# Kernel tuning notes

Measured on AMD Instinct MI355X. Metric: run time of the kernel, lower is better.

## Reference

```python
import jax, jax.numpy as jnp
import numpy as np

L, H, D, E, F, T, B, V = 6, 6, 64, 384, 1536, 256, 256, 65


def setup_inputs() -> dict:
    key = jax.random.key(0)
    ks = iter(jax.random.split(key, 32))
    s = 0.02
    n = lambda shape: jax.random.normal(next(ks), shape, dtype=jnp.float32) * s
    inp = {
        "inputs": jax.random.randint(next(ks), (B, T), 0, V),
        "targets": jax.random.randint(next(ks), (B, T), 0, V),
        "tok_emb": n((V, E)),
        "pos_emb": n((T, E)),
        "Wq": n((L, H, E, D)),
        "Wk": n((L, H, E, D)),
        "Wv": n((L, H, E, D)),
        "Wo": n((L, E, E)),
        "bo": jnp.zeros((L, E), jnp.float32),
        "ln1_g": jnp.ones((L, E), jnp.float32),
        "ln1_b": jnp.zeros((L, E), jnp.float32),
        "W1": n((L, E, F)),
        "b1": jnp.zeros((L, F), jnp.float32),
        "W2": n((L, F, E)),
        "b2": jnp.zeros((L, E), jnp.float32),
        "ln2_g": jnp.ones((L, E), jnp.float32),
        "ln2_b": jnp.zeros((L, E), jnp.float32),
        "lnf_g": jnp.ones((E,), jnp.float32),
        "lnf_b": jnp.zeros((E,), jnp.float32),
        "Wh": n((E, V)),
        "bh": jnp.zeros((V,), jnp.float32),
    }
    return inp


def _layer_norm(x, g, b, eps=1e-5):
    mu = jnp.mean(x, axis=-1, keepdims=True)
    var = jnp.var(x, axis=-1, keepdims=True)
    return (x - mu) * jax.lax.rsqrt(var + eps) * g + b


def _forward(inputs, targets, tok_emb, pos_emb, Wq, Wk, Wv, Wo, bo,
             ln1_g, ln1_b, W1, b1, W2, b2, ln2_g, ln2_b, lnf_g, lnf_b, Wh, bh):
    Bc, Tc = inputs.shape
    x = tok_emb[inputs] + pos_emb[:Tc]  # [B,T,E]
    causal = jnp.tril(jnp.ones((Tc, Tc), bool))
    scale = D ** -0.5
    for l in range(L):
        h = _layer_norm(x, ln1_g[l], ln1_b[l])
        q = jnp.einsum('bte,hed->bhtd', h, Wq[l])
        k = jnp.einsum('bte,hed->bhtd', h, Wk[l])
        v = jnp.einsum('bte,hed->bhtd', h, Wv[l])
        scores = jnp.einsum('bhtd,bhsd->bhts', q, k) * scale
        scores = jnp.where(causal, scores, -jnp.inf)
        att = jax.nn.softmax(scores, axis=-1)
        o = jnp.einsum('bhts,bhsd->bhtd', att, v)
        o = o.transpose(0, 2, 1, 3).reshape(Bc, Tc, E)  # concat heads
        x = x + o @ Wo[l] + bo[l]
        h2 = _layer_norm(x, ln2_g[l], ln2_b[l])
        x = x + jax.nn.relu(h2 @ W1[l] + b1[l]) @ W2[l] + b2[l]
    x = _layer_norm(x, lnf_g, lnf_b)
    logits = x @ Wh + bh  # [B,T,V]
    logp = jax.nn.log_softmax(logits, axis=-1)
    nll = -jnp.take_along_axis(logp, targets[..., None], axis=-1)[..., 0]
    loss = jnp.mean(nll)
    return logits.reshape(Bc * Tc, V), loss


def reference(inputs, targets, tok_emb, pos_emb, Wq, Wk, Wv, Wo, bo,
              ln1_g, ln1_b, W1, b1, W2, b2, ln2_g, ln2_b, lnf_g, lnf_b, Wh, bh):
    return _forward(inputs, targets, tok_emb, pos_emb, Wq, Wk, Wv, Wo, bo,
                    ln1_g, ln1_b, W1, b1, W2, b2, ln2_g, ln2_b, lnf_g, lnf_b, Wh, bh)
```

## Files before the change

kernel.cpp:

```cpp
#include <hip/hip_runtime.h>
#include <math.h>

#define LL 6
#define HH 6
#define EE 384
#define FF 1536
#define TT 256
#define BB 256
#define VV 65
constexpr int BT = BB * TT;

typedef __attribute__((ext_vector_type(8))) short s16x8;
typedef __attribute__((ext_vector_type(4))) float f32x4;
typedef __attribute__((ext_vector_type(2))) unsigned int u32x2;
typedef unsigned int uint;
typedef unsigned short ushort_t;

__device__ __forceinline__ float uaf(uint u) { union { uint u; float f; } c; c.u = u; return c.f; }
__device__ __forceinline__ ushort_t f2b(float f) {
  union { float f; uint u; } c; c.f = f;
  uint r = c.u + 0x7fffu + ((c.u >> 16) & 1u);
  return (ushort_t)(r >> 16);
}
__device__ __forceinline__ float b2f(ushort_t b) { return uaf((uint)b << 16); }

__device__ __forceinline__ void gload_lds16(const void* g, void* l) {
  __builtin_amdgcn_global_load_lds(
      (const __attribute__((address_space(1))) unsigned int*)g,
      (__attribute__((address_space(3))) unsigned int*)l, 16, 0, 0);
}

__global__ __launch_bounds__(256)
void embed_kernel(const int* __restrict__ inp, const float* __restrict__ tok,
                  const float* __restrict__ pos, float* __restrict__ x) {
  int idx = blockIdx.x * 256 + threadIdx.x;
  int e4 = idx % (EE / 4);
  int r = idx / (EE / 4);
  int t = r % TT;
  int tk = inp[r];
  float4 a = ((const float4*)tok)[tk * (EE / 4) + e4];
  float4 p = ((const float4*)pos)[t * (EE / 4) + e4];
  float4 o;
  o.x = a.x + p.x; o.y = a.y + p.y; o.z = a.z + p.z; o.w = a.w + p.w;
  ((float4*)x)[idx] = o;
}

__global__ __launch_bounds__(256)
void pack_qkv(const float* __restrict__ Wq, const float* __restrict__ Wk,
              const float* __restrict__ Wv, ushort_t* __restrict__ dst) {
  int idx = blockIdx.x * 256 + threadIdx.x;
  int l = idx / (1152 * 384);
  int r = idx % (1152 * 384);
  int n = r / 384;
  int k = r % 384;
  int which = n / 384;
  int hd = n % 384;
  int h = hd >> 6, d = hd & 63;
  const float* src = which == 0 ? Wq : (which == 1 ? Wk : Wv);
  dst[idx] = f2b(src[((size_t)(l * HH + h) * EE + k) * 64 + d]);
}

__global__ __launch_bounds__(256)
void pack_wt(const float* __restrict__ src, ushort_t* __restrict__ dst, int Kd, int Nd) {
  int idx = blockIdx.x * 256 + threadIdx.x;
  int l = idx / (Kd * Nd);
  int r = idx % (Kd * Nd);
  int n = r / Kd;
  int k = r % Kd;
  dst[idx] = f2b(src[((size_t)l * Kd + k) * Nd + n]);
}

__global__ __launch_bounds__(256)
void pack_head(const float* __restrict__ Wh, ushort_t* __restrict__ dst) {
  int idx = blockIdx.x * 256 + threadIdx.x;
  int n = idx / 384, k = idx % 384;
  dst[idx] = (n < VV) ? f2b(Wh[(size_t)k * VV + n]) : (ushort_t)0;
}

__global__ __launch_bounds__(256)
void layernorm_384(const float* __restrict__ x, const float* __restrict__ g,
                   const float* __restrict__ b, ushort_t* __restrict__ outp) {
  int wid = threadIdx.x >> 6, lane = threadIdx.x & 63;
  int row = blockIdx.x * 4 + wid;
  const float* xr = x + (size_t)row * EE;
  float v[6];
  float s = 0.f, s2 = 0.f;
#pragma unroll
  for (int i = 0; i < 6; ++i) {
    v[i] = xr[lane + 64 * i];
    s += v[i];
    s2 += v[i] * v[i];
  }
#pragma unroll
  for (int off = 32; off; off >>= 1) {
    s += __shfl_xor(s, off);
    s2 += __shfl_xor(s2, off);
  }
  float mu = s * (1.f / EE);
  float var = s2 * (1.f / EE) - mu * mu;
  float rs = rsqrtf(var + 1e-5f);
#pragma unroll
  for (int i = 0; i < 6; ++i) {
    int e = lane + 64 * i;
    outp[(size_t)row * EE + e] = f2b((v[i] - mu) * rs * g[e] + b[e]);
  }
}

__global__ __launch_bounds__(256)
void ln_res_384(float* __restrict__ x, const ushort_t* __restrict__ delta,
                const float* __restrict__ g, const float* __restrict__ b,
                ushort_t* __restrict__ outp) {
  int wid = threadIdx.x >> 6, lane = threadIdx.x & 63;
  int row = blockIdx.x * 4 + wid;
  float* xr = x + (size_t)row * EE;
  const ushort_t* dr = delta + (size_t)row * EE;
  float v[6];
  float s = 0.f, s2 = 0.f;
#pragma unroll
  for (int i = 0; i < 6; ++i) {
    int e = lane + 64 * i;
    v[i] = xr[e] + b2f(dr[e]);
    s += v[i];
    s2 += v[i] * v[i];
  }
#pragma unroll
  for (int off = 32; off; off >>= 1) {
    s += __shfl_xor(s, off);
    s2 += __shfl_xor(s2, off);
  }
  float mu = s * (1.f / EE);
  float var = s2 * (1.f / EE) - mu * mu;
  float rs = rsqrtf(var + 1e-5f);
#pragma unroll
  for (int i = 0; i < 6; ++i) {
    int e = lane + 64 * i;
    xr[e] = v[i];
    outp[(size_t)row * EE + e] = f2b((v[i] - mu) * rs * g[e] + b[e]);
  }
}

template <int MODE, bool BIAS, bool RELU>
__global__ __launch_bounds__(256)
void gemm_bf16(const ushort_t* __restrict__ A, const ushort_t* __restrict__ Wt,
               const float* __restrict__ bias, ushort_t* __restrict__ Cb,
               float* __restrict__ Cf, ushort_t* __restrict__ Cv,
               int M, int N, int K, int nx) {
  __shared__ ushort_t sm[16896];
  ushort_t* As = sm;
  ushort_t* Bs = sm + 8192;
  const int tid = threadIdx.x;

  int bid = blockIdx.x;
  {
    const int nwg = gridDim.x;
    const int q = nwg >> 3, rr = nwg & 7;
    const int xcd = bid & 7, within = bid >> 3;
    bid = (xcd < rr ? xcd * (q + 1) : rr * (q + 1) + (xcd - rr) * q) + within;
  }
  const int bn = (bid % nx) * 128;
  const int bm = (bid / nx) * 128;

  const int w = tid >> 6, lane = tid & 63;
  const int wr = (w >> 1) * 64, wc = (w & 1) * 64;
  const int fr = lane & 15, fq = lane >> 4;

  const int rp = lane >> 2;
  const int fqs = (lane & 3) ^ ((rp >> 1) & 3);
  const ushort_t* Ag0 = A + (size_t)(bm + w * 16 + rp) * K + fqs * 8;
  const ushort_t* Ag1 = Ag0 + (size_t)64 * K;
  const ushort_t* Bg0 = Wt + (size_t)(bn + w * 16 + rp) * K + fqs * 8;
  const ushort_t* Bg1 = Bg0 + (size_t)64 * K;

  const int slotr = (fq ^ ((fr >> 1) & 3)) * 8;
  const ushort_t* Ard = As + (wr + fr) * 32 + slotr;
  const ushort_t* Brd = Bs + (wc + fr) * 32 + slotr;

  const int nt = K >> 5;
  auto STAGE = [&](int kt, int b) {
    const int k0 = kt << 5;
    const int bo = b << 12;
    gload_lds16(Ag0 + k0, As + bo + (w * 16) * 32);
    gload_lds16(Ag1 + k0, As + bo + (64 + w * 16) * 32);
    gload_lds16(Bg0 + k0, Bs + bo + (w * 16) * 32);
    gload_lds16(Bg1 + k0, Bs + bo + (64 + w * 16) * 32);
  };

  f32x4 acc[4][4] = {};
  STAGE(0, 0);

  for (int t = 0; t < nt; ++t) {
    const int bo = (t & 1) << 12;
    if (t + 1 < nt) {
      STAGE(t + 1, (t & 1) ^ 1);
      asm volatile("s_waitcnt vmcnt(4)" ::: "memory");
    } else {
      asm volatile("s_waitcnt vmcnt(0)" ::: "memory");
    }
    __builtin_amdgcn_s_barrier();
    __builtin_amdgcn_sched_barrier(0);
    s16x8 afr[4], bfr[4];
#pragma unroll
    for (int m = 0; m < 4; ++m) afr[m] = *(const s16x8*)(Ard + bo + m * 512);
#pragma unroll
    for (int n = 0; n < 4; ++n) bfr[n] = *(const s16x8*)(Brd + bo + n * 512);
#pragma unroll
    for (int m = 0; m < 4; ++m)
#pragma unroll
      for (int n = 0; n < 4; ++n)
        acc[m][n] = __builtin_amdgcn_mfma_f32_16x16x32_bf16(afr[m], bfr[n], acc[m][n], 0, 0, 0);
    __builtin_amdgcn_sched_barrier(0);
    __builtin_amdgcn_s_barrier();
  }

  if constexpr (MODE == 0 || MODE == 3) {
    if (MODE == 3 && bn >= 768) {
      const int r0 = bm + wr + fq * 4;
      const int c0 = bn + wc + fr;
#pragma unroll
      for (int n = 0; n < 4; ++n) {
        const int col = c0 + n * 16 - 768;
#pragma unroll
        for (int m = 0; m < 4; ++m) {
          const int row = r0 + m * 16;
          uint lo = (uint)f2b(acc[m][n][0]) | ((uint)f2b(acc[m][n][1]) << 16);
          uint hi = (uint)f2b(acc[m][n][2]) | ((uint)f2b(acc[m][n][3]) << 16);
          *(u32x2*)&Cv[(size_t)col * M + row] = u32x2{lo, hi};
        }
      }
      return;
    }
    const int ostride = (MODE == 3) ? 768 : N;
#pragma unroll
    for (int n = 0; n < 4; ++n) {
      const int col = wc + n * 16 + fr;
      const float bv = BIAS ? bias[bn + col] : 0.f;
#pragma unroll
      for (int m = 0; m < 4; ++m) {
        const int row = wr + m * 16 + fq * 4;
#pragma unroll
        for (int j = 0; j < 4; ++j) {
          float vv = acc[m][n][j] + bv;
          if constexpr (RELU) vv = fmaxf(vv, 0.f);
          sm[(row + j) * 132 + col] = f2b(vv);
        }
      }
    }
    __syncthreads();
    const int rr2 = tid >> 4, cb = (tid & 15) * 8;
#pragma unroll
    for (int pp = 0; pp < 8; ++pp) {
      const int row = pp * 16 + rr2;
      s16x8 v8 = *(const s16x8*)(sm + row * 132 + cb);
      *(s16x8*)(Cb + (size_t)(bm + row) * ostride + bn + cb) = v8;
    }
    return;
  }
  const int r0 = bm + wr + fq * 4;
  const int c0 = bn + wc + fr;
#pragma unroll
  for (int n = 0; n < 4; ++n) {
    const int col = c0 + n * 16;
    if (col >= VV) continue;
    const float bv = BIAS ? bias[col] : 0.f;
#pragma unroll
    for (int m = 0; m < 4; ++m) {
      const int row = r0 + m * 16;
#pragma unroll
      for (int j = 0; j < 4; ++j)
        Cf[(size_t)(row + j) * VV + col] = acc[m][n][j] + bv;
    }
  }
}

__global__ __launch_bounds__(256)
void attn_kernel(const ushort_t* __restrict__ qk, const ushort_t* __restrict__ vt,
                 ushort_t* __restrict__ o, int R) {
  __shared__ ushort_t Ks[256 * 64];
  __shared__ ushort_t Pb[4][16 * 40];
  const int tid = threadIdx.x;
  const int w = tid >> 6, lane = tid & 63;
  const int seq = blockIdx.x / HH, hh = blockIdx.x % HH;
  const int brow = seq * TT;

  {
    const ushort_t* kbase = qk + (size_t)brow * 768 + 384 + hh * 64;
#pragma unroll
    for (int cc = 0; cc < 8; ++cc) {
      const int ci = cc * 256 + tid;
      const int s = ci >> 3, j = ci & 7;
      const int srcb = (j * 16) ^ ((s & 7) << 4);
      gload_lds16(kbase + (size_t)s * 768 + (srcb >> 1), Ks + cc * 2048 + w * 512);
    }
  }
  __syncthreads();

  const int r = lane & 15, g = lane >> 4;
  ushort_t* pw = &Pb[w][0];

  for (int fi = 0; fi < 4; ++fi) {
    const int q0 = fi * 64 + w * 16;
    const int n_st = (q0 >> 4) + 1;
    const ushort_t* qrow = qk + (size_t)(brow + q0 + r) * 768 + hh * 64 + g * 8;
    const s16x8 qa0 = *(const s16x8*)qrow;
    const s16x8 qa1 = *(const s16x8*)(qrow + 32);

    f32x4 S[16];
#pragma unroll
    for (int st = 0; st < 16; ++st) {
      if (st < n_st) {
        const int srow = st * 16 + r;
        const int sw = (srow & 7) << 4;
        const s16x8 kb0 = *(const s16x8*)(Ks + ((srow * 128 + ((g * 16) ^ sw)) >> 1));
        const s16x8 kb1 = *(const s16x8*)(Ks + ((srow * 128 + ((64 + g * 16) ^ sw)) >> 1));
        f32x4 t = {0.f, 0.f, 0.f, 0.f};
        t = __builtin_amdgcn_mfma_f32_16x16x32_bf16(qa0, kb0, t, 0, 0, 0);
        t = __builtin_amdgcn_mfma_f32_16x16x32_bf16(qa1, kb1, t, 0, 0, 0);
        if (st == n_st - 1) {
#pragma unroll
          for (int j = 0; j < 4; ++j)
            t[j] = (r <= g * 4 + j) ? t[j] : -1e30f;
        }
        S[st] = t;
      }
    }

    float mrow[4] = {-1e30f, -1e30f, -1e30f, -1e30f};
#pragma unroll
    for (int st = 0; st < 16; ++st)
      if (st < n_st) {
#pragma unroll
        for (int j = 0; j < 4; ++j) mrow[j] = fmaxf(mrow[j], S[st][j]);
      }
#pragma unroll
    for (int j = 0; j < 4; ++j) {
      float m = mrow[j];
      m = fmaxf(m, __shfl_xor(m, 1));
      m = fmaxf(m, __shfl_xor(m, 2));
      m = fmaxf(m, __shfl_xor(m, 4));
      m = fmaxf(m, __shfl_xor(m, 8));
      mrow[j] = m;
    }

    float rsum[4] = {0.f, 0.f, 0.f, 0.f};
    f32x4 O[4] = {f32x4{0,0,0,0}, f32x4{0,0,0,0}, f32x4{0,0,0,0}, f32x4{0,0,0,0}};
    const int n_sc = (n_st + 1) >> 1;
    const ushort_t* vbase = vt + (size_t)(hh * 64 + r) * R + brow + g * 8;
#pragma unroll
    for (int sc = 0; sc < 8; ++sc) {
      if (sc < n_sc) {
#pragma unroll
        for (int tt = 0; tt < 2; ++tt) {
          const int st = sc * 2 + tt;
#pragma unroll
          for (int j = 0; j < 4; ++j) {
            float p = 0.f;
            if (st < n_st) p = __expf((S[st][j] - mrow[j]) * 0.125f);
            rsum[j] += p;
            pw[((g * 4 + j) * 80 + tt * 32 + r * 2) >> 1] = f2b(p);
          }
        }
        asm volatile("s_waitcnt lgkmcnt(0)" ::: "memory");
        __builtin_amdgcn_sched_barrier(0);
        const s16x8 pa = *(const s16x8*)(pw + ((r * 80 + g * 16) >> 1));
#pragma unroll
        for (int dt = 0; dt < 4; ++dt) {
          const s16x8 vb = *(const s16x8*)(vbase + (size_t)dt * 16 * R + sc * 32);
          O[dt] = __builtin_amdgcn_mfma_f32_16x16x32_bf16(pa, vb, O[dt], 0, 0, 0);
        }
      }
    }

#pragma unroll
    for (int j = 0; j < 4; ++j) {
      float s = rsum[j];
      s += __shfl_xor(s, 1);
      s += __shfl_xor(s, 2);
      s += __shfl_xor(s, 4);
      s += __shfl_xor(s, 8);
      rsum[j] = 1.f / s;
    }
    ushort_t* obase = o + (size_t)(brow + q0 + g * 4) * 384 + hh * 64 + r;
#pragma unroll
    for (int j = 0; j < 4; ++j)
#pragma unroll
      for (int dt = 0; dt < 4; ++dt)
        obase[(size_t)j * 384 + dt * 16] = f2b(O[dt][j] * rsum[j]);
  }
}

__global__ __launch_bounds__(256)
void loss_kernel(const float* __restrict__ logits, const int* __restrict__ targets,
                 float* __restrict__ loss_acc, int R) {
  __shared__ float red[4];
  int wid = threadIdx.x >> 6, lane = threadIdx.x & 63;
  float lsum = 0.f;
  for (int r = blockIdx.x * 4 + wid; r < R; r += gridDim.x * 4) {
    const float* lrow = logits + (size_t)r * VV;
    float v = lrow[lane];
    float e64 = lrow[64];
    float m = fmaxf(v, e64);
#pragma unroll
    for (int off = 32; off; off >>= 1) m = fmaxf(m, __shfl_xor(m, off));
    float s = expf(v - m);
#pragma unroll
    for (int off = 32; off; off >>= 1) s += __shfl_xor(s, off);
    s += expf(e64 - m);
    float lse = m + logf(s);
    int t = targets[r];
    float tv = (t < 64) ? __shfl(v, t) : e64;
    lsum += lse - tv;
  }
  if (lane == 0) red[wid] = lsum;
  __syncthreads();
  if (threadIdx.x == 0)
    atomicAdd(loss_acc, (red[0] + red[1] + red[2] + red[3]) * (1.f / BT));
}

extern "C" void kernel_launch(void* const* d_in, const int* in_sizes, int n_in,
                              void* d_out, int out_size, void* d_ws, size_t ws_size,
                              hipStream_t stream) {
  const int* inputs = (const int*)d_in[0];
  const int* targets = (const int*)d_in[1];
  const float* tok_emb = (const float*)d_in[2];
  const float* pos_emb = (const float*)d_in[3];
  const float* Wq = (const float*)d_in[4];
  const float* Wk = (const float*)d_in[5];
  const float* Wv = (const float*)d_in[6];
  const float* Wo = (const float*)d_in[7];
  const float* bo = (const float*)d_in[8];
  const float* ln1_g = (const float*)d_in[9];
  const float* ln1_b = (const float*)d_in[10];
  const float* W1 = (const float*)d_in[11];
  const float* b1 = (const float*)d_in[12];
  const float* W2 = (const float*)d_in[13];
  const float* b2 = (const float*)d_in[14];
  const float* ln2_g = (const float*)d_in[15];
  const float* ln2_b = (const float*)d_in[16];
  const float* lnf_g = (const float*)d_in[17];
  const float* lnf_b = (const float*)d_in[18];
  const float* Wh = (const float*)d_in[19];
  const float* bh = (const float*)d_in[20];

  float* logits = (float*)d_out;
  float* loss = logits + (size_t)BT * VV;

  auto al = [](size_t b) { return (b + 255) & ~(size_t)255; };
  const size_t wq_b = al((size_t)LL * 1152 * 384 * 2);
  const size_t wo_b = al((size_t)LL * 384 * 384 * 2);
  const size_t w1_b = al((size_t)LL * 1536 * 384 * 2);
  const size_t wh_b = al((size_t)128 * 384 * 2);
  const size_t wfix = wq_b + wo_b + 2 * w1_b + wh_b;

  int c = BB;
  while (c > 1 && wfix + (size_t)c * 256 * 6144 > ws_size) c >>= 1;
  const int R = c * TT;
  const int nch = BB / c;

  char* p = (char*)d_ws;
  ushort_t* wqkv = (ushort_t*)p; p += wq_b;
  ushort_t* wot  = (ushort_t*)p; p += wo_b;
  ushort_t* w1t  = (ushort_t*)p; p += w1_b;
  ushort_t* w2t  = (ushort_t*)p; p += w1_b;
  ushort_t* whb  = (ushort_t*)p; p += wh_b;
  float* x = (float*)p;          p += (size_t)R * 1536;
  ushort_t* hb = (ushort_t*)p;   p += (size_t)R * 768;
  ushort_t* ob = (ushort_t*)p;   p += (size_t)R * 768;
  ushort_t* un = (ushort_t*)p;
  ushort_t* qkb = un;
  ushort_t* vtb = un + (size_t)R * 768;
  ushort_t* midb = un;

  hipMemsetAsync(loss, 0, 4, stream);
  pack_qkv<<<LL * 1152 * 384 / 256, 256, 0, stream>>>(Wq, Wk, Wv, wqkv);
  pack_wt<<<LL * 384 * 384 / 256, 256, 0, stream>>>(Wo, wot, 384, 384);
  pack_wt<<<LL * 384 * 1536 / 256, 256, 0, stream>>>(W1, w1t, 384, 1536);
  pack_wt<<<LL * 1536 * 384 / 256, 256, 0, stream>>>(W2, w2t, 1536, 384);
  pack_head<<<128 * 384 / 256, 256, 0, stream>>>(Wh, whb);

  const int my = R / 128;
  for (int ch = 0; ch < nch; ++ch) {
    const size_t r0 = (size_t)ch * R;
    embed_kernel<<<R * 96 / 256, 256, 0, stream>>>(inputs + r0, tok_emb, pos_emb, x);
    layernorm_384<<<R / 4, 256, 0, stream>>>(x, ln1_g, ln1_b, hb);
    for (int l = 0; l < LL; ++l) {
      gemm_bf16<3, false, false><<<9 * my, 256, 0, stream>>>(
          hb, wqkv + (size_t)l * 1152 * 384, nullptr, qkb, nullptr, vtb, R, 1152, 384, 9);
      attn_kernel<<<c * HH, 256, 0, stream>>>(qkb, vtb, ob, R);
      gemm_bf16<0, true, false><<<3 * my, 256, 0, stream>>>(
          ob, wot + (size_t)l * 384 * 384, bo + l * EE, hb, nullptr, nullptr, R, 384, 384, 3);
      ln_res_384<<<R / 4, 256, 0, stream>>>(x, hb, ln2_g + l * EE, ln2_b + l * EE, hb);
      gemm_bf16<0, true, true><<<12 * my, 256, 0, stream>>>(
          hb, w1t + (size_t)l * 1536 * 384, b1 + l * FF, midb, nullptr, nullptr, R, 1536, 384, 12);
      gemm_bf16<0, true, false><<<3 * my, 256, 0, stream>>>(
          midb, w2t + (size_t)l * 384 * 1536, b2 + l * EE, hb, nullptr, nullptr, R, 384, 1536, 3);
      if (l + 1 < LL)
        ln_res_384<<<R / 4, 256, 0, stream>>>(x, hb, ln1_g + (l + 1) * EE,
                                              ln1_b + (l + 1) * EE, hb);
      else
        ln_res_384<<<R / 4, 256, 0, stream>>>(x, hb, lnf_g, lnf_b, hb);
    }
    gemm_bf16<2, true, false><<<1 * my, 256, 0, stream>>>(
        hb, whb, bh, nullptr, logits + r0 * VV, nullptr, R, 128, 384, 1);
    loss_kernel<<<1024, 256, 0, stream>>>(logits + r0 * VV, targets + r0, loss, R);
  }
}
```

Measured before the change: 3.336 ms.

## Stage V in LDS and balance causal query tiles across eight waves

The attention kernel now runs with 512 threads (8 waves). Each block stages the head's full V^T slice into shared memory with a padded row stride, so the PV MFMA operands come from LDS instead of repeated global loads. Each wave handles query tiles w and 15-w, which balances the causal workload across waves. The explicit lgkmcnt wait and sched barrier before reading the P tile are dropped. Shared memory use rises to about 75 KB per block, which limits occupancy, and the 258-element row stride gives 16-byte LDS vector accesses that are not 16-byte aligned.

```diff
diff --git a/kernel.cpp b/kernel.cpp
--- a/kernel.cpp
+++ b/kernel.cpp
@@ -272,11 +272,12 @@
   }
 }
 
-__global__ __launch_bounds__(256)
+__global__ __launch_bounds__(512, 4)
 void attn_kernel(const ushort_t* __restrict__ qk, const ushort_t* __restrict__ vt,
                  ushort_t* __restrict__ o, int R) {
-  __shared__ ushort_t Ks[256 * 64];
-  __shared__ ushort_t Pb[4][16 * 40];
+  __shared__ ushort_t Ks[16384];
+  __shared__ ushort_t Vs[16512];
+  __shared__ ushort_t Pb[8][640];
   const int tid = threadIdx.x;
   const int w = tid >> 6, lane = tid & 63;
   const int seq = blockIdx.x / HH, hh = blockIdx.x % HH;
@@ -285,21 +286,37 @@
   {
     const ushort_t* kbase = qk + (size_t)brow * 768 + 384 + hh * 64;
 #pragma unroll
-    for (int cc = 0; cc < 8; ++cc) {
-      const int ci = cc * 256 + tid;
+    for (int cc = 0; cc < 4; ++cc) {
+      const int ci = cc * 512 + tid;
       const int s = ci >> 3, j = ci & 7;
       const int srcb = (j * 16) ^ ((s & 7) << 4);
-      gload_lds16(kbase + (size_t)s * 768 + (srcb >> 1), Ks + cc * 2048 + w * 512);
-    }
+      gload_lds16(kbase + (size_t)s * 768 + (srcb >> 1), Ks + cc * 4096 + w * 512);
+    }
+  }
+  {
+    s16x8 vreg[4];
+    int vidx[4];
+#pragma unroll
+    for (int t2 = 0; t2 < 4; ++t2) {
+      const int ci = t2 * 512 + tid;
+      const int d = ci >> 5, c2 = ci & 31;
+      vidx[t2] = d * 258 + c2 * 8;
+      vreg[t2] = *(const s16x8*)(vt + (size_t)(hh * 64 + d) * R + brow + c2 * 8);
+    }
+#pragma unroll
+    for (int t2 = 0; t2 < 4; ++t2)
+      *(s16x8*)(Vs + vidx[t2]) = vreg[t2];
   }
   __syncthreads();
 
   const int r = lane & 15, g = lane >> 4;
   ushort_t* pw = &Pb[w][0];
 
-  for (int fi = 0; fi < 4; ++fi) {
-    const int q0 = fi * 64 + w * 16;
-    const int n_st = (q0 >> 4) + 1;
+#pragma unroll
+  for (int qti = 0; qti < 2; ++qti) {
+    const int qt = qti ? (15 - w) : w;
+    const int q0 = qt << 4;
+    const int n_st = qt + 1;
     const ushort_t* qrow = qk + (size_t)(brow + q0 + r) * 768 + hh * 64 + g * 8;
     const s16x8 qa0 = *(const s16x8*)qrow;
     const s16x8 qa1 = *(const s16x8*)(qrow + 32);
@@ -344,7 +361,6 @@
     float rsum[4] = {0.f, 0.f, 0.f, 0.f};
     f32x4 O[4] = {f32x4{0,0,0,0}, f32x4{0,0,0,0}, f32x4{0,0,0,0}, f32x4{0,0,0,0}};
     const int n_sc = (n_st + 1) >> 1;
-    const ushort_t* vbase = vt + (size_t)(hh * 64 + r) * R + brow + g * 8;
 #pragma unroll
     for (int sc = 0; sc < 8; ++sc) {
       if (sc < n_sc) {
@@ -356,15 +372,13 @@
             float p = 0.f;
             if (st < n_st) p = __expf((S[st][j] - mrow[j]) * 0.125f);
             rsum[j] += p;
-            pw[((g * 4 + j) * 80 + tt * 32 + r * 2) >> 1] = f2b(p);
+            pw[(g * 4 + j) * 40 + tt * 16 + r] = f2b(p);
           }
         }
-        asm volatile("s_waitcnt lgkmcnt(0)" ::: "memory");
-        __builtin_amdgcn_sched_barrier(0);
-        const s16x8 pa = *(const s16x8*)(pw + ((r * 80 + g * 16) >> 1));
+        const s16x8 pa = *(const s16x8*)(pw + r * 40 + g * 8);
 #pragma unroll
         for (int dt = 0; dt < 4; ++dt) {
-          const s16x8 vb = *(const s16x8*)(vbase + (size_t)dt * 16 * R + sc * 32);
+          const s16x8 vb = *(const s16x8*)(Vs + (dt * 16 + r) * 258 + sc * 32 + g * 8);
           O[dt] = __builtin_amdgcn_mfma_f32_16x16x32_bf16(pa, vb, O[dt], 0, 0, 0);
         }
       }
@@ -485,7 +499,7 @@
     for (int l = 0; l < LL; ++l) {
       gemm_bf16<3, false, false><<<9 * my, 256, 0, stream>>>(
           hb, wqkv + (size_t)l * 1152 * 384, nullptr, qkb, nullptr, vtb, R, 1152, 384, 9);
-      attn_kernel<<<c * HH, 256, 0, stream>>>(qkb, vtb, ob, R);
+      attn_kernel<<<c * HH, 512, 0, stream>>>(qkb, vtb, ob, R);
       gemm_bf16<0, true, false><<<3 * my, 256, 0, stream>>>(
           ob, wot + (size_t)l * 384 * 384, bo + l * EE, hb, nullptr, nullptr, R, 384, 384, 3);
       ln_res_384<<<R / 4, 256, 0, stream>>>(x, hb, ln2_g + l * EE, ln2_b + l * EE, hb);
```

Measured after the change: 3.073 ms. 1.09x faster.
